# Kernel tuning notes

Measured on AMD Instinct MI355X. Metric: run time of the kernel, lower is better.

The kernel has to match this reference:

```python
import jax, jax.numpy as jnp
import numpy as np
import math

B, N, D, H, A, OBS, NB = 256, 64, 512, 8, 64, 128, 4
HD = D // H
EPS = 1e-5


def layernorm(x, g, b):
    mu = jnp.mean(x, axis=-1, keepdims=True)
    var = jnp.mean((x - mu) ** 2, axis=-1, keepdims=True)
    return (x - mu) * jax.lax.rsqrt(var + EPS) * g + b


def gelu(x):
    return jax.nn.gelu(x, approximate=False)  # torch nn.GELU default = exact erf


def mha_masked(k_in, v_in, q_in, wq, wk, wv, wp, bq, bk, bv, bp):
    # weights stored [in, out]; torch Linear computes x @ W.T, same math with random init
    b, l, d = q_in.shape
    q = (q_in @ wq + bq).reshape(b, l, H, HD).transpose(0, 2, 1, 3)  # [B,H,L,hd]
    k = (k_in @ wk + bk).reshape(b, l, H, HD).transpose(0, 2, 1, 3)
    v = (v_in @ wv + bv).reshape(b, l, H, HD).transpose(0, 2, 1, 3)
    att = jnp.einsum('bhqd,bhkd->bhqk', q, k) * (1.0 / math.sqrt(HD))
    causal = jnp.tril(jnp.ones((l, l), dtype=bool))  # registered tril buffer in original MAT code
    att = jnp.where(causal[None, None], att, -jnp.inf)
    att = jax.nn.softmax(att, axis=-1)
    y = jnp.einsum('bhqk,bhkd->bhqd', att, v)
    y = y.transpose(0, 2, 1, 3).reshape(b, l, d)
    return y @ wp + bp


def setup_inputs() -> dict:
    key = jax.random.key(0)
    ks = iter(jax.random.split(key, 32))
    s = 0.02
    inp = {
        'action': jax.random.normal(next(ks), (B, N, A + 1), jnp.float32),
        'obs_rep': jax.random.normal(next(ks), (B, N, D), jnp.float32),
        'obs': jax.random.normal(next(ks), (B, N, OBS), jnp.float32),
        'w_ae': jax.random.normal(next(ks), (A + 1, D), jnp.float32) * s,
        'ln0_g': jnp.ones((D,), jnp.float32),
        'ln0_b': jnp.zeros((D,), jnp.float32),
        'blk_ln_g': jnp.ones((NB, 3, D), jnp.float32),
        'blk_ln_b': jnp.zeros((NB, 3, D), jnp.float32),
        'blk_wq': jax.random.normal(next(ks), (NB, 2, D, D), jnp.float32) * s,
        'blk_wk': jax.random.normal(next(ks), (NB, 2, D, D), jnp.float32) * s,
        'blk_wv': jax.random.normal(next(ks), (NB, 2, D, D), jnp.float32) * s,
        'blk_wp': jax.random.normal(next(ks), (NB, 2, D, D), jnp.float32) * s,
        'blk_bq': jnp.zeros((NB, 2, D), jnp.float32),
        'blk_bk': jnp.zeros((NB, 2, D), jnp.float32),
        'blk_bv': jnp.zeros((NB, 2, D), jnp.float32),
        'blk_bp': jnp.zeros((NB, 2, D), jnp.float32),
        'blk_w1': jax.random.normal(next(ks), (NB, D, D), jnp.float32) * s,
        'blk_b1': jnp.zeros((NB, D), jnp.float32),
        'blk_w2': jax.random.normal(next(ks), (NB, D, D), jnp.float32) * s,
        'blk_b2': jnp.zeros((NB, D), jnp.float32),
        'wh1': jax.random.normal(next(ks), (D, D), jnp.float32) * s,
        'bh1': jnp.zeros((D,), jnp.float32),
        'lnh_g': jnp.ones((D,), jnp.float32),
        'lnh_b': jnp.zeros((D,), jnp.float32),
        'wh2': jax.random.normal(next(ks), (D, A), jnp.float32) * s,
        'bh2': jnp.zeros((A,), jnp.float32),
    }
    return inp


def reference(action, obs_rep, obs, w_ae, ln0_g, ln0_b, blk_ln_g, blk_ln_b,
              blk_wq, blk_wk, blk_wv, blk_wp, blk_bq, blk_bk, blk_bv, blk_bp,
              blk_w1, blk_b1, blk_w2, blk_b2, wh1, bh1, lnh_g, lnh_b, wh2, bh2):
    # action encoder: Linear(no bias) + GELU, then LayerNorm
    x = layernorm(gelu(action @ w_ae), ln0_g, ln0_b)
    for i in range(NB):
        # sublayer 1: masked self-attn + residual + LN
        a1 = mha_masked(x, x, x, blk_wq[i, 0], blk_wk[i, 0], blk_wv[i, 0], blk_wp[i, 0],
                        blk_bq[i, 0], blk_bk[i, 0], blk_bv[i, 0], blk_bp[i, 0])
        x = layernorm(x + a1, blk_ln_g[i, 0], blk_ln_b[i, 0])
        # sublayer 2: masked cross-attn (key=x, value=x, query=obs_rep) + residual with obs_rep + LN
        a2 = mha_masked(x, x, obs_rep, blk_wq[i, 1], blk_wk[i, 1], blk_wv[i, 1], blk_wp[i, 1],
                        blk_bq[i, 1], blk_bk[i, 1], blk_bv[i, 1], blk_bp[i, 1])
        x = layernorm(obs_rep + a2, blk_ln_g[i, 1], blk_ln_b[i, 1])
        # sublayer 3: GELU MLP (D -> D -> D) + residual + LN
        m = gelu(x @ blk_w1[i] + blk_b1[i]) @ blk_w2[i] + blk_b2[i]
        x = layernorm(x + m, blk_ln_g[i, 2], blk_ln_b[i, 2])
    # head: Linear + GELU + LN + Linear
    h = layernorm(gelu(x @ wh1 + bh1), lnh_g, lnh_b)
    logit = h @ wh2 + bh2
    return logit
```

## Files before the change

### kernel.cpp

```cpp
#include <hip/hip_runtime.h>
#include <hip/hip_bf16.h>
#include <math.h>

namespace {

constexpr int B  = 256;
constexpr int N  = 64;
constexpr int D  = 512;
constexpr int H  = 8;
constexpr int NBLK = 4;
constexpr int M  = B * N;
constexpr float EPS = 1e-5f;
constexpr float SCALE = 0.125f;
constexpr int NEVER = 1 << 20;

typedef __attribute__((ext_vector_type(8))) short short8b;
typedef __attribute__((ext_vector_type(4))) float f32x4;

__device__ __forceinline__ float gelu_exact(float x) {
  return 0.5f * x * (1.0f + erff(x * 0.70710678118654752440f));
}

__device__ __forceinline__ unsigned short f2b_bits(float f) {
  __hip_bfloat16 h = __float2bfloat16(f);
  return *reinterpret_cast<unsigned short*>(&h);
}

#define GLOBAL_AS __attribute__((address_space(1)))
#define LDS_AS    __attribute__((address_space(3)))

__device__ __forceinline__ void gload_lds16(const void* g, void* l) {
  __builtin_amdgcn_global_load_lds((const GLOBAL_AS void*)g, (LDS_AS void*)l, 16, 0, 0);
}

template<bool GELU, int SPLIT>
__global__ __launch_bounds__(512, 2) void gemm_dp_kernel(
    const __hip_bfloat16* __restrict__ A,
    const __hip_bfloat16* __restrict__ Wt,
    const float* __restrict__ bias,
    __hip_bfloat16* __restrict__ out1, int ostr1,
    __hip_bfloat16* __restrict__ vt, int gy) {
  constexpr int K = 512;
  constexpr int NT = 8;
  __shared__ __hip_bfloat16 Als[3][128][64];
  __shared__ __hip_bfloat16 Bls[3][256][64];

  const int nwg = gridDim.x;
  const int hw  = blockIdx.x;
  const int cpx = nwg >> 3;
  const int lg  = (hw & 7) * cpx + (hw >> 3);
  const int bm  = (lg / gy) * 128;
  const int bn  = (lg % gy) * 256;

  const int tid  = threadIdx.x;
  const int wave = tid >> 6;
  const int lane = tid & 63;
  const int wm   = (wave >> 2) * 64;
  const int wn   = (wave & 3) * 64;
  const int fr   = lane & 15;
  const int fg   = lane >> 4;

  const int srow  = tid >> 3;
  const int sslot = (tid & 7) ^ (srow & 7);
  const __hip_bfloat16* gA = A  + (size_t)(bm + srow) * K + sslot * 8;
  const __hip_bfloat16* gB = Wt + (size_t)(bn + srow) * K + sslot * 8;

  auto STAGE = [&](int buf, int kt) {
    const int ko = kt * 64;
    char* la = (char*)&Als[buf][0][0] + wave * 1024;
    char* lb = (char*)&Bls[buf][0][0] + wave * 1024;
    gload_lds16(gA + ko,           la);
    gload_lds16(gA + 64 * K + ko,  la + 8192);
    gload_lds16(gB + ko,           lb);
    gload_lds16(gB + 64 * K + ko,  lb + 8192);
    gload_lds16(gB + 128 * K + ko, lb + 16384);
    gload_lds16(gB + 192 * K + ko, lb + 24576);
  };

  auto lda = [&](int buf, int mi, int ks) -> short8b {
    const int row  = wm + mi * 16 + fr;
    const int byte = row * 128 + (((ks << 2) | fg) ^ (fr & 7)) * 16;
    return *reinterpret_cast<const short8b*>((const char*)&Als[buf][0][0] + byte);
  };
  auto ldb = [&](int buf, int ni, int ks) -> short8b {
    const int row  = wn + ni * 16 + fr;
    const int byte = row * 128 + (((ks << 2) | fg) ^ (fr & 7)) * 16;
    return *reinterpret_cast<const short8b*>((const char*)&Bls[buf][0][0] + byte);
  };

  STAGE(0, 0);
  STAGE(1, 1);
  asm volatile("s_waitcnt vmcnt(6)" ::: "memory");
  __builtin_amdgcn_sched_barrier(0);
  __builtin_amdgcn_s_barrier();
  __builtin_amdgcn_sched_barrier(0);

  f32x4 acc[4][4] = {};
  for (int t = 0; t < NT; ++t) {
    const int cur = t % 3;
    if (t + 2 < NT) STAGE((t + 2) % 3, t + 2);

    short8b a0[4], b0[4], a1[4], b1[4];
#pragma unroll
    for (int mi = 0; mi < 4; ++mi) a0[mi] = lda(cur, mi, 0);
#pragma unroll
    for (int ni = 0; ni < 4; ++ni) b0[ni] = ldb(cur, ni, 0);
#pragma unroll
    for (int mi = 0; mi < 4; ++mi) a1[mi] = lda(cur, mi, 1);
#pragma unroll
    for (int ni = 0; ni < 4; ++ni) b1[ni] = ldb(cur, ni, 1);

    __builtin_amdgcn_s_setprio(1);
#pragma unroll
    for (int mi = 0; mi < 4; ++mi)
#pragma unroll
      for (int ni = 0; ni < 4; ++ni)
        acc[mi][ni] = __builtin_amdgcn_mfma_f32_16x16x32_bf16(a0[mi], b0[ni], acc[mi][ni], 0, 0, 0);
#pragma unroll
    for (int mi = 0; mi < 4; ++mi)
#pragma unroll
      for (int ni = 0; ni < 4; ++ni)
        acc[mi][ni] = __builtin_amdgcn_mfma_f32_16x16x32_bf16(a1[mi], b1[ni], acc[mi][ni], 0, 0, 0);
    __builtin_amdgcn_s_setprio(0);

    if (t + 2 < NT) {
      asm volatile("s_waitcnt vmcnt(6)" ::: "memory");
    } else {
      asm volatile("s_waitcnt vmcnt(0)" ::: "memory");
    }
    __builtin_amdgcn_sched_barrier(0);
    __builtin_amdgcn_s_barrier();
    __builtin_amdgcn_sched_barrier(0);
  }

#pragma unroll
  for (int ni = 0; ni < 4; ++ni) {
    const int col = bn + wn + ni * 16 + fr;
    const float bv = bias ? bias[col] : 0.f;
#pragma unroll
    for (int mi = 0; mi < 4; ++mi) {
      const int row0 = bm + wm + mi * 16 + fg * 4;
      if (col >= SPLIT) {
        const int vcol = col - SPLIT;
        ushort4 o;
        o.x = f2b_bits(acc[mi][ni][0] + bv);
        o.y = f2b_bits(acc[mi][ni][1] + bv);
        o.z = f2b_bits(acc[mi][ni][2] + bv);
        o.w = f2b_bits(acc[mi][ni][3] + bv);
        const int b8 = row0 >> 6, nl = row0 & 63;
        const int hh = vcol >> 6, dl = vcol & 63;
        *reinterpret_cast<ushort4*>(vt +
            ((size_t)(b8 * 8 + hh) * 4096 + dl * 64 + nl)) = o;
      } else {
#pragma unroll
        for (int q = 0; q < 4; ++q) {
          float v = acc[mi][ni][q] + bv;
          if (GELU) v = gelu_exact(v);
          out1[(size_t)(row0 + q) * ostr1 + col] = __float2bfloat16(v);
        }
      }
    }
  }
}

template<int KSTEPS>
__global__ __launch_bounds__(256) void gemm_head_kernel(
    const __hip_bfloat16* __restrict__ A,
    const __hip_bfloat16* __restrict__ Wt,
    const float* __restrict__ bias,
    float* __restrict__ out1, int ostr1, int nvalid) {
  constexpr int K = KSTEPS * 32;
  __shared__ __hip_bfloat16 Als[2][128][32];
  __shared__ __hip_bfloat16 Bls[2][128][32];

  const int bm   = blockIdx.x * 128;
  const int bn   = blockIdx.y * 128;
  const int tid  = threadIdx.x;
  const int wave = tid >> 6;
  const int lane = tid & 63;
  const int wm   = (wave >> 1) * 64;
  const int wn   = (wave & 1) * 64;
  const int fr   = lane & 15;
  const int fg   = lane >> 4;

  const int srow = (lane >> 2);
  const int scol = (lane & 3) * 8;
  const __hip_bfloat16* gA0 = A  + (size_t)(bm + wave * 32 + srow) * K + scol;
  const __hip_bfloat16* gA1 = gA0 + 16 * K;
  const __hip_bfloat16* gB0 = Wt + (size_t)(bn + wave * 32 + srow) * K + scol;
  const __hip_bfloat16* gB1 = gB0 + 16 * K;

  f32x4 acc[4][4] = {};

  auto stage = [&](int buf, int ks) {
    const int ko = ks * 32;
    gload_lds16(gA0 + ko, &Als[buf][wave * 32][0]);
    gload_lds16(gA1 + ko, &Als[buf][wave * 32 + 16][0]);
    gload_lds16(gB0 + ko, &Bls[buf][wave * 32][0]);
    gload_lds16(gB1 + ko, &Bls[buf][wave * 32 + 16][0]);
  };

  stage(0, 0);
  int buf = 0;
  for (int ks = 0; ks < KSTEPS; ++ks) {
    __syncthreads();
    if (ks + 1 < KSTEPS) stage(buf ^ 1, ks + 1);
    short8b a[4], b[4];
#pragma unroll
    for (int mi = 0; mi < 4; ++mi)
      a[mi] = *reinterpret_cast<const short8b*>(&Als[buf][wm + mi * 16 + fr][fg * 8]);
#pragma unroll
    for (int ni = 0; ni < 4; ++ni)
      b[ni] = *reinterpret_cast<const short8b*>(&Bls[buf][wn + ni * 16 + fr][fg * 8]);
#pragma unroll
    for (int mi = 0; mi < 4; ++mi)
#pragma unroll
      for (int ni = 0; ni < 4; ++ni)
        acc[mi][ni] = __builtin_amdgcn_mfma_f32_16x16x32_bf16(a[mi], b[ni], acc[mi][ni], 0, 0, 0);
    buf ^= 1;
  }

#pragma unroll
  for (int ni = 0; ni < 4; ++ni) {
    const int col = bn + wn + ni * 16 + fr;
    if (col >= nvalid) continue;
    const float bv = bias ? bias[col] : 0.f;
#pragma unroll
    for (int mi = 0; mi < 4; ++mi) {
      const int row0 = bm + wm + mi * 16 + fg * 4;
#pragma unroll
      for (int q = 0; q < 4; ++q)
        out1[(size_t)(row0 + q) * ostr1 + col] = acc[mi][ni][q] + bv;
    }
  }
}

template<int KSTEPS, bool GELU_PRE, bool RES>
__global__ __launch_bounds__(512) void gemm_ln_kernel(
    const __hip_bfloat16* __restrict__ A,
    const __hip_bfloat16* __restrict__ Wt,
    const float* __restrict__ bias,
    const __hip_bfloat16* __restrict__ resb,
    const float* __restrict__ g, const float* __restrict__ bb,
    __hip_bfloat16* __restrict__ outB) {
  constexpr int K = KSTEPS * 32;
  __shared__ __hip_bfloat16 Als[2][64][32];
  __shared__ __hip_bfloat16 Bls[2][512][32];
  __shared__ float red[64][8];
  __shared__ float mrow[64];
  __shared__ float rrow[64];

  const int bm   = blockIdx.x * 64;
  const int tid  = threadIdx.x;
  const int wave = tid >> 6;
  const int lane = tid & 63;
  const int fr   = lane & 15;
  const int fg   = lane >> 4;
  const int srow = lane >> 2;
  const int scol = (lane & 3) * 8;

  auto stage = [&](int buf, int ks) {
    const int ko = ks * 32;
    if (wave < 4)
      gload_lds16(A + (size_t)(bm + wave * 16 + srow) * K + ko + scol,
                  &Als[buf][wave * 16][0]);
#pragma unroll
    for (int c = 0; c < 4; ++c)
      gload_lds16(Wt + (size_t)(wave * 64 + c * 16 + srow) * K + ko + scol,
                  &Bls[buf][wave * 64 + c * 16][0]);
  };

  f32x4 acc[4][4] = {};
  stage(0, 0);
  int buf = 0;
  for (int ks = 0; ks < KSTEPS; ++ks) {
    __syncthreads();
    if (ks + 1 < KSTEPS) stage(buf ^ 1, ks + 1);
    short8b a[4], b[4];
#pragma unroll
    for (int mi = 0; mi < 4; ++mi)
      a[mi] = *reinterpret_cast<const short8b*>(&Als[buf][mi * 16 + fr][fg * 8]);
#pragma unroll
    for (int ni = 0; ni < 4; ++ni)
      b[ni] = *reinterpret_cast<const short8b*>(&Bls[buf][wave * 64 + ni * 16 + fr][fg * 8]);
#pragma unroll
    for (int mi = 0; mi < 4; ++mi)
#pragma unroll
      for (int ni = 0; ni < 4; ++ni)
        acc[mi][ni] = __builtin_amdgcn_mfma_f32_16x16x32_bf16(a[mi], b[ni], acc[mi][ni], 0, 0, 0);
    buf ^= 1;
  }

  float v[4][4][4];
  float bvc[4];
#pragma unroll
  for (int ni = 0; ni < 4; ++ni)
    bvc[ni] = bias ? bias[wave * 64 + ni * 16 + fr] : 0.f;
#pragma unroll
  for (int mi = 0; mi < 4; ++mi)
#pragma unroll
    for (int q = 0; q < 4; ++q) {
      const int row = bm + mi * 16 + fg * 4 + q;
#pragma unroll
      for (int ni = 0; ni < 4; ++ni) {
        float t = acc[mi][ni][q] + bvc[ni];
        if (GELU_PRE) t = gelu_exact(t);
        if (RES)
          t += __bfloat162float(resb[(size_t)row * D + wave * 64 + ni * 16 + fr]);
        v[mi][ni][q] = t;
      }
    }

  float ps[16];
#pragma unroll
  for (int mi = 0; mi < 4; ++mi)
#pragma unroll
    for (int q = 0; q < 4; ++q)
      ps[mi * 4 + q] = v[mi][0][q] + v[mi][1][q] + v[mi][2][q] + v[mi][3][q];
#pragma unroll
  for (int mask = 1; mask < 16; mask <<= 1)
#pragma unroll
    for (int t = 0; t < 16; ++t) ps[t] += __shfl_xor(ps[t], mask);
  if (fr == 0) {
#pragma unroll
    for (int mi = 0; mi < 4; ++mi)
#pragma unroll
      for (int q = 0; q < 4; ++q)
        red[mi * 16 + fg * 4 + q][wave] = ps[mi * 4 + q];
  }
  __syncthreads();
  if (tid < 64) {
    float s = 0.f;
#pragma unroll
    for (int w = 0; w < 8; ++w) s += red[tid][w];
    mrow[tid] = s * (1.f / 512.f);
  }
  __syncthreads();
  float mu[16];
#pragma unroll
  for (int mi = 0; mi < 4; ++mi)
#pragma unroll
    for (int q = 0; q < 4; ++q) mu[mi * 4 + q] = mrow[mi * 16 + fg * 4 + q];

  float ps2[16];
#pragma unroll
  for (int mi = 0; mi < 4; ++mi)
#pragma unroll
    for (int q = 0; q < 4; ++q) {
      const float m = mu[mi * 4 + q];
      float s = 0.f;
#pragma unroll
      for (int ni = 0; ni < 4; ++ni) {
        const float d = v[mi][ni][q] - m;
        s += d * d;
      }
      ps2[mi * 4 + q] = s;
    }
#pragma unroll
  for (int mask = 1; mask < 16; mask <<= 1)
#pragma unroll
    for (int t = 0; t < 16; ++t) ps2[t] += __shfl_xor(ps2[t], mask);
  if (fr == 0) {
#pragma unroll
    for (int mi = 0; mi < 4; ++mi)
#pragma unroll
      for (int q = 0; q < 4; ++q)
        red[mi * 16 + fg * 4 + q][wave] = ps2[mi * 4 + q];
  }
  __syncthreads();
  if (tid < 64) {
    float s = 0.f;
#pragma unroll
    for (int w = 0; w < 8; ++w) s += red[tid][w];
    rrow[tid] = rsqrtf(s * (1.f / 512.f) + EPS);
  }
  __syncthreads();

#pragma unroll
  for (int ni = 0; ni < 4; ++ni) {
    const int col = wave * 64 + ni * 16 + fr;
    const float gc = g[col], bc = bb[col];
#pragma unroll
    for (int mi = 0; mi < 4; ++mi)
#pragma unroll
      for (int q = 0; q < 4; ++q) {
        const int lrow = mi * 16 + fg * 4 + q;
        const int row = bm + lrow;
        const float o = (v[mi][ni][q] - mu[mi * 4 + q]) * rrow[lrow] * gc + bc;
        outB[(size_t)row * D + col] = __float2bfloat16(o);
      }
  }
}

__global__ __launch_bounds__(256) void attn_mfma_kernel(
    const __hip_bfloat16* __restrict__ qg, int qstr,
    const __hip_bfloat16* __restrict__ kg, int kstr,
    const __hip_bfloat16* __restrict__ vt,
    __hip_bfloat16* __restrict__ yg) {
  __shared__ __align__(16) char smem[33280];
  unsigned short* Qs  = (unsigned short*)smem;
  unsigned short* Ks  = (unsigned short*)(smem + 8192);
  float*          Ss  = (float*)smem;
  unsigned short* Vts = (unsigned short*)(smem + 16896);
  unsigned short* Ps  = (unsigned short*)(smem + 25088);

  const int tid  = threadIdx.x;
  const int bh   = blockIdx.x;
  const int bidx = bh >> 3, h = bh & 7;
  const size_t rbase = (size_t)bidx * 64;
  const int col0 = h * 64;

  const __hip_bfloat16* vtg = vt + (size_t)bh * 4096;
#pragma unroll
  for (int p = 0; p < 2; ++p) {
    const int idx = tid + p * 256;
    const int row = idx >> 3, c8 = (idx & 7) * 8;
    const int lb  = (row * 128 + c8 * 2) ^ ((row & 7) << 4);
    const uint4 vq = *reinterpret_cast<const uint4*>(qg + (rbase + row) * qstr + col0 + c8);
    const uint4 vk = *reinterpret_cast<const uint4*>(kg + (rbase + row) * kstr + col0 + c8);
    const uint4 vv = *reinterpret_cast<const uint4*>(vtg + idx * 8);
    *reinterpret_cast<uint4*>((char*)Qs  + lb) = vq;
    *reinterpret_cast<uint4*>((char*)Ks  + lb) = vk;
    *reinterpret_cast<uint4*>((char*)Vts + lb) = vv;
  }
  __syncthreads();

  const int wave = tid >> 6, lane = tid & 63;
  const int fr = lane & 15, fg = lane >> 4;
  const int wr = (wave >> 1) * 32, wc = (wave & 1) * 32;

  auto ldfrag = [&](const unsigned short* base, int row, int ks) -> short8b {
    const int byte = (row * 128 + ks * 64 + fg * 16) ^ ((row & 7) << 4);
    return *reinterpret_cast<const short8b*>((const char*)base + byte);
  };

  f32x4 acc[2][2] = {};
#pragma unroll
  for (int ks = 0; ks < 2; ++ks) {
    short8b a[2], b[2];
    a[0] = ldfrag(Qs, wr + fr, ks);
    a[1] = ldfrag(Qs, wr + 16 + fr, ks);
    b[0] = ldfrag(Ks, wc + fr, ks);
    b[1] = ldfrag(Ks, wc + 16 + fr, ks);
#pragma unroll
    for (int mi = 0; mi < 2; ++mi)
#pragma unroll
      for (int ni = 0; ni < 2; ++ni)
        acc[mi][ni] = __builtin_amdgcn_mfma_f32_16x16x32_bf16(a[mi], b[ni], acc[mi][ni], 0, 0, 0);
  }
  __syncthreads();

#pragma unroll
  for (int mi = 0; mi < 2; ++mi)
#pragma unroll
    for (int ni = 0; ni < 2; ++ni) {
      const int m2 = wc + ni * 16 + fr;
#pragma unroll
      for (int r = 0; r < 4; ++r) {
        const int n = wr + mi * 16 + fg * 4 + r;
        Ss[n * 66 + m2] = (m2 <= n) ? acc[mi][ni][r] * SCALE : -1e30f;
      }
    }
  __syncthreads();

  for (int n = wave * 16; n < wave * 16 + 16; ++n) {
    const float vv = Ss[n * 66 + lane];
    float mx = vv;
#pragma unroll
    for (int off = 1; off < 64; off <<= 1) mx = fmaxf(mx, __shfl_xor(mx, off));
    const float p = (lane <= n) ? __expf(vv - mx) : 0.f;
    float sum = p;
#pragma unroll
    for (int off = 1; off < 64; off <<= 1) sum += __shfl_xor(sum, off);
    const int byte = (n * 128 + lane * 2) ^ ((n & 7) << 4);
    *(unsigned short*)((char*)Ps + byte) = f2b_bits(p / sum);
  }
  __syncthreads();

  f32x4 acc2[2][2] = {};
#pragma unroll
  for (int ks = 0; ks < 2; ++ks) {
    short8b a[2], b[2];
    a[0] = ldfrag(Ps, wr + fr, ks);
    a[1] = ldfrag(Ps, wr + 16 + fr, ks);
    b[0] = ldfrag(Vts, wc + fr, ks);
    b[1] = ldfrag(Vts, wc + 16 + fr, ks);
#pragma unroll
    for (int mi = 0; mi < 2; ++mi)
#pragma unroll
      for (int ni = 0; ni < 2; ++ni)
        acc2[mi][ni] = __builtin_amdgcn_mfma_f32_16x16x32_bf16(a[mi], b[ni], acc2[mi][ni], 0, 0, 0);
  }
#pragma unroll
  for (int mi = 0; mi < 2; ++mi)
#pragma unroll
    for (int r = 0; r < 4; ++r) {
      const int n = wr + mi * 16 + fg * 4 + r;
      yg[(rbase + n) * 512 + col0 + wc + fr]      = __float2bfloat16(acc2[mi][0][r]);
      yg[(rbase + n) * 512 + col0 + wc + 16 + fr] = __float2bfloat16(acc2[mi][1][r]);
    }
}

__global__ __launch_bounds__(256) void wconv_all_kernel(
    const float* __restrict__ bwq, const float* __restrict__ bwk,
    const float* __restrict__ bwv, const float* __restrict__ bwp,
    const float* __restrict__ bw1, const float* __restrict__ bw2,
    const float* __restrict__ wh1,
    __hip_bfloat16* __restrict__ wSelf, __hip_bfloat16* __restrict__ wCq,
    __hip_bfloat16* __restrict__ wCkv, __hip_bfloat16* __restrict__ wTp,
    __hip_bfloat16* __restrict__ wTw1, __hip_bfloat16* __restrict__ wTw2,
    __hip_bfloat16* __restrict__ wTh1) {
  const size_t MAT = (size_t)D * D;
  const size_t SS = (size_t)1536 * 512, KV = (size_t)1024 * 512;
  const int z = blockIdx.z;
  const float* src;
  __hip_bfloat16* dst;
  if (z < 8)       { int i = z >> 1; src = bwq + (size_t)z * MAT;
                     dst = (z & 1) ? wCq + (size_t)i * MAT : wSelf + (size_t)i * SS; }
  else if (z < 16) { int zz = z - 8, i = zz >> 1; src = bwk + (size_t)zz * MAT;
                     dst = (zz & 1) ? wCkv + (size_t)i * KV
                                    : wSelf + (size_t)i * SS + 512 * 512; }
  else if (z < 24) { int zz = z - 16, i = zz >> 1; src = bwv + (size_t)zz * MAT;
                     dst = (zz & 1) ? wCkv + (size_t)i * KV + 512 * 512
                                    : wSelf + (size_t)i * SS + 1024 * 512; }
  else if (z < 32) { int zz = z - 24; src = bwp + (size_t)zz * MAT; dst = wTp + (size_t)zz * MAT; }
  else if (z < 36) { int zz = z - 32; src = bw1 + (size_t)zz * MAT; dst = wTw1 + (size_t)zz * MAT; }
  else if (z < 40) { int zz = z - 36; src = bw2 + (size_t)zz * MAT; dst = wTw2 + (size_t)zz * MAT; }
  else             { src = wh1; dst = wTh1; }

  __shared__ float tile[32][33];
  const int r0 = blockIdx.y * 32, c0 = blockIdx.x * 32;
  const int tr = threadIdx.x >> 5;
  const int tc = threadIdx.x & 31;
#pragma unroll
  for (int i = 0; i < 4; ++i)
    tile[tr + 8 * i][tc] = src[(size_t)(r0 + tr + 8 * i) * D + c0 + tc];
  __syncthreads();
#pragma unroll
  for (int i = 0; i < 4; ++i)
    dst[(size_t)(c0 + tr + 8 * i) * D + r0 + tc] = __float2bfloat16(tile[tc][tr + 8 * i]);
}

__global__ __launch_bounds__(256) void misc_prep_kernel(
    const float* __restrict__ w_ae, const float* __restrict__ wh2,
    const float* __restrict__ bbq, const float* __restrict__ bbk,
    const float* __restrict__ bbv, const float* __restrict__ action,
    __hip_bfloat16* __restrict__ waeT, __hip_bfloat16* __restrict__ wh2p,
    float* __restrict__ selfb, float* __restrict__ ckvb,
    float* __restrict__ bqc, __hip_bfloat16* __restrict__ actb) {
  constexpr int R0 = 512 * 96, R1 = 128 * 512, R2 = NBLK * 1536,
                R3 = NBLK * 1024, R4 = NBLK * 512, R5 = M * 96;
  constexpr int total = R0 + R1 + R2 + R3 + R4 + R5;
  for (int i = blockIdx.x * 256 + threadIdx.x; i < total; i += gridDim.x * 256) {
    int j = i;
    if (j < R0) {
      const int n = j / 96, k = j - n * 96;
      waeT[j] = (k < 65) ? __float2bfloat16(w_ae[(size_t)k * 512 + n]) : __float2bfloat16(0.f);
    } else if ((j -= R0) < R1) {
      const int n = j >> 9, k = j & 511;
      wh2p[j] = (n < 64) ? __float2bfloat16(wh2[(size_t)k * 64 + n]) : __float2bfloat16(0.f);
    } else if ((j -= R1) < R2) {
      const int blk = j / 1536, c = j - blk * 1536;
      const int seg = c >> 9, cc = c & 511;
      const float* s = (seg == 0) ? bbq : (seg == 1) ? bbk : bbv;
      selfb[j] = s[(size_t)(blk * 2) * 512 + cc];
    } else if ((j -= R2) < R3) {
      const int blk = j >> 10, c = j & 1023;
      ckvb[j] = (c < 512) ? bbk[(size_t)(blk * 2 + 1) * 512 + c]
                          : bbv[(size_t)(blk * 2 + 1) * 512 + (c - 512)];
    } else if ((j -= R3) < R4) {
      const int blk = j >> 9, c = j & 511;
      bqc[j] = bbq[(size_t)(blk * 2 + 1) * 512 + c];
    } else {
      j -= R4;
      const int row = j / 96, k = j - row * 96;
      actb[j] = (k < 65) ? __float2bfloat16(action[(size_t)row * 65 + k]) : __float2bfloat16(0.f);
    }
  }
}

__global__ __launch_bounds__(256) void cvt_kernel(
    const float* __restrict__ src, __hip_bfloat16* __restrict__ dst, int n4) {
  const int i = blockIdx.x * 256 + threadIdx.x;
  if (i < n4) {
    const float4 v = reinterpret_cast<const float4*>(src)[i];
    ushort4 o;
    o.x = f2b_bits(v.x); o.y = f2b_bits(v.y);
    o.z = f2b_bits(v.z); o.w = f2b_bits(v.w);
    reinterpret_cast<ushort4*>(dst)[i] = o;
  }
}

}

extern "C" void kernel_launch(void* const* d_in, const int* in_sizes, int n_in,
                              void* d_out, int out_size, void* d_ws, size_t ws_size,
                              hipStream_t stream) {
  const float* action  = (const float*)d_in[0];
  const float* obs_rep = (const float*)d_in[1];
  const float* w_ae    = (const float*)d_in[3];
  const float* ln0_g   = (const float*)d_in[4];
  const float* ln0_b   = (const float*)d_in[5];
  const float* bln_g   = (const float*)d_in[6];
  const float* bln_b   = (const float*)d_in[7];
  const float* bwq     = (const float*)d_in[8];
  const float* bwk     = (const float*)d_in[9];
  const float* bwv     = (const float*)d_in[10];
  const float* bwp     = (const float*)d_in[11];
  const float* bbq     = (const float*)d_in[12];
  const float* bbk     = (const float*)d_in[13];
  const float* bbv     = (const float*)d_in[14];
  const float* bbp     = (const float*)d_in[15];
  const float* bw1     = (const float*)d_in[16];
  const float* bb1     = (const float*)d_in[17];
  const float* bw2     = (const float*)d_in[18];
  const float* bb2     = (const float*)d_in[19];
  const float* wh1     = (const float*)d_in[20];
  const float* bh1     = (const float*)d_in[21];
  const float* lnh_g   = (const float*)d_in[22];
  const float* lnh_b   = (const float*)d_in[23];
  const float* wh2     = (const float*)d_in[24];
  const float* bh2     = (const float*)d_in[25];

  char* ws = (char*)d_ws;
  const size_t MAT = (size_t)D * D;
  const size_t szB = (size_t)M * D * 2;

  __hip_bfloat16* xb  = (__hip_bfloat16*)ws; ws += szB;
  __hip_bfloat16* hb  = (__hip_bfloat16*)ws; ws += szB;
  __hip_bfloat16* vtb = (__hip_bfloat16*)ws; ws += szB;
  __hip_bfloat16* orb = (__hip_bfloat16*)ws; ws += szB;
  __hip_bfloat16* qkb = (__hip_bfloat16*)ws; ws += 2 * szB;
  __hip_bfloat16* qcb = (__hip_bfloat16*)ws; ws += 4 * szB;
  __hip_bfloat16* kb  = (__hip_bfloat16*)ws; ws += szB;
  __hip_bfloat16* actb = (__hip_bfloat16*)ws; ws += (size_t)M * 96 * 2;
  __hip_bfloat16* wSelf = (__hip_bfloat16*)ws; ws += (size_t)NBLK * 1536 * 512 * 2;
  __hip_bfloat16* wCq   = (__hip_bfloat16*)ws; ws += (size_t)NBLK * 512 * 512 * 2;
  __hip_bfloat16* wCkv  = (__hip_bfloat16*)ws; ws += (size_t)NBLK * 1024 * 512 * 2;
  __hip_bfloat16* wTp   = (__hip_bfloat16*)ws; ws += 8 * MAT * 2;
  __hip_bfloat16* wTw1  = (__hip_bfloat16*)ws; ws += 4 * MAT * 2;
  __hip_bfloat16* wTw2  = (__hip_bfloat16*)ws; ws += 4 * MAT * 2;
  __hip_bfloat16* wTh1  = (__hip_bfloat16*)ws; ws += MAT * 2;
  __hip_bfloat16* wh2p  = (__hip_bfloat16*)ws; ws += 128 * 512 * 2;
  __hip_bfloat16* waeT  = (__hip_bfloat16*)ws; ws += 512 * 96 * 2;
  float* selfb         = (float*)ws;         ws += (size_t)NBLK * 1536 * 4;
  float* ckvb          = (float*)ws;         ws += (size_t)NBLK * 1024 * 4;
  float* bqc           = (float*)ws;         ws += (size_t)NBLK * 512 * 4;

  wconv_all_kernel<<<dim3(16, 16, 41), 256, 0, stream>>>(
      bwq, bwk, bwv, bwp, bw1, bw2, wh1,
      wSelf, wCq, wCkv, wTp, wTw1, wTw2, wTh1);
  misc_prep_kernel<<<2048, 256, 0, stream>>>(
      w_ae, wh2, bbq, bbk, bbv, action, waeT, wh2p, selfb, ckvb, bqc, actb);
  cvt_kernel<<<(M * D / 4 + 255) / 256, 256, 0, stream>>>(obs_rep, orb, M * D / 4);

  const size_t SS = (size_t)1536 * 512;
  const size_t KV = (size_t)1024 * 512;
  const int lnGrid = M / 64;

  gemm_ln_kernel<3, true, false><<<lnGrid, 512, 0, stream>>>(
      actb, waeT, nullptr, nullptr, ln0_g, ln0_b, xb);

  gemm_dp_kernel<false, NEVER><<<M / 128 * 8, 512, 0, stream>>>(
      orb, wCq, bqc, qcb, 2048, nullptr, 8);

  for (int i = 0; i < NBLK; ++i) {
    const float* g0 = bln_g + (size_t)(i * 3 + 0) * D;
    const float* b0 = bln_b + (size_t)(i * 3 + 0) * D;
    const float* g1 = bln_g + (size_t)(i * 3 + 1) * D;
    const float* b1 = bln_b + (size_t)(i * 3 + 1) * D;
    const float* g2 = bln_g + (size_t)(i * 3 + 2) * D;
    const float* b2 = bln_b + (size_t)(i * 3 + 2) * D;

    gemm_dp_kernel<false, 1024><<<M / 128 * 6, 512, 0, stream>>>(
        xb, wSelf + (size_t)i * SS, selfb + (size_t)i * 1536, qkb, 1024, vtb, 6);
    attn_mfma_kernel<<<B * H, 256, 0, stream>>>(qkb, 1024, qkb + 512, 1024, vtb, hb);
    gemm_ln_kernel<16, false, true><<<lnGrid, 512, 0, stream>>>(
        hb, wTp + (size_t)(i * 2) * MAT, bbp + (size_t)(i * 2) * D, xb, g0, b0, xb);

    gemm_dp_kernel<false, 512><<<M / 128 * 4, 512, 0, stream>>>(
        xb, wCkv + (size_t)i * KV, ckvb + (size_t)i * 1024, kb, 512, vtb, 4);
    attn_mfma_kernel<<<B * H, 256, 0, stream>>>(
        qcb + (size_t)i * 512, 2048, kb, 512, vtb, hb);
    gemm_ln_kernel<16, false, true><<<lnGrid, 512, 0, stream>>>(
        hb, wTp + (size_t)(i * 2 + 1) * MAT, bbp + (size_t)(i * 2 + 1) * D,
        orb, g1, b1, xb);

    gemm_dp_kernel<true, NEVER><<<M / 128 * 2, 512, 0, stream>>>(
        xb, wTw1 + (size_t)i * MAT, bb1 + (size_t)i * D, hb, 512, nullptr, 2);
    gemm_ln_kernel<16, false, true><<<lnGrid, 512, 0, stream>>>(
        hb, wTw2 + (size_t)i * MAT, bb2 + (size_t)i * D, xb, g2, b2, xb);
  }

  gemm_ln_kernel<16, true, false><<<lnGrid, 512, 0, stream>>>(
      xb, wTh1, bh1, nullptr, lnh_g, lnh_b, hb);
  gemm_head_kernel<16><<<dim3(M / 128, 1), 256, 0, stream>>>(
      hb, wh2p, bh2, (float*)d_out, 64, 64);
}
```

Before: 1.039 ms.

## Use 64-wide K tiles with XOR-swizzled LDS in fused GEMM+LayerNorm kernels

Adds a gemm_ln64 kernel for the K=512 GEMM+LayerNorm stages. It stages 64-wide K tiles into LDS using an XOR swizzle to avoid bank conflicts, halves the number of barrier-separated iterations, and raises wave priority around the MFMA block. The encoder gets a specialised small-K kernel, and the obs_rep fp32-to-bf16 conversion moves into misc_prep_kernel, which saves one launch. The larger tiles roughly double LDS use per block, which may lower occupancy.

```diff
diff --git a/kernel.cpp b/kernel.cpp
--- a/kernel.cpp
+++ b/kernel.cpp
@@ -163,6 +163,184 @@
   }
 }
 
+template<bool GELU_PRE, bool RES>
+__global__ __launch_bounds__(512) void gemm_ln64_kernel(
+    const __hip_bfloat16* __restrict__ A,
+    const __hip_bfloat16* __restrict__ Wt,
+    const float* __restrict__ bias,
+    const __hip_bfloat16* __restrict__ resb,
+    const float* __restrict__ g, const float* __restrict__ bb,
+    __hip_bfloat16* __restrict__ outB) {
+  __shared__ __hip_bfloat16 Als[2][64][64];
+  __shared__ __hip_bfloat16 Bls[2][512][64];
+  __shared__ float red[64][8];
+  __shared__ float mrow[64];
+  __shared__ float rrow[64];
+
+  const int bm   = blockIdx.x * 64;
+  const int tid  = threadIdx.x;
+  const int wave = tid >> 6;
+  const int lane = tid & 63;
+  const int fr   = lane & 15;
+  const int fg   = lane >> 4;
+
+  const int srow  = tid >> 3;
+  const int sslot = (tid & 7) ^ (srow & 7);
+
+  auto stage = [&](int buf, int kt) {
+    const int ko = kt * 64;
+    gload_lds16(A + (size_t)(bm + srow) * 512 + ko + sslot * 8,
+                (char*)&Als[buf][0][0] + wave * 1024);
+#pragma unroll
+    for (int j = 0; j < 8; ++j) {
+      const int row = j * 64 + srow;
+      const int sl  = (tid & 7) ^ (row & 7);
+      gload_lds16(Wt + (size_t)row * 512 + ko + sl * 8,
+                  (char*)&Bls[buf][0][0] + j * 8192 + wave * 1024);
+    }
+  };
+
+  auto lda = [&](int buf, int mi, int ks) -> short8b {
+    const int row  = mi * 16 + fr;
+    const int byte = row * 128 + (((ks << 2) | fg) ^ (row & 7)) * 16;
+    return *reinterpret_cast<const short8b*>((const char*)&Als[buf][0][0] + byte);
+  };
+  auto ldb = [&](int buf, int ni, int ks) -> short8b {
+    const int row  = wave * 64 + ni * 16 + fr;
+    const int byte = row * 128 + (((ks << 2) | fg) ^ (row & 7)) * 16;
+    return *reinterpret_cast<const short8b*>((const char*)&Bls[buf][0][0] + byte);
+  };
+
+  f32x4 acc[4][4] = {};
+  stage(0, 0);
+  int buf = 0;
+  for (int kt = 0; kt < 8; ++kt) {
+    __syncthreads();
+    if (kt + 1 < 8) stage(buf ^ 1, kt + 1);
+    short8b a0[4], b0[4], a1[4], b1[4];
+#pragma unroll
+    for (int mi = 0; mi < 4; ++mi) a0[mi] = lda(buf, mi, 0);
+#pragma unroll
+    for (int ni = 0; ni < 4; ++ni) b0[ni] = ldb(buf, ni, 0);
+#pragma unroll
+    for (int mi = 0; mi < 4; ++mi) a1[mi] = lda(buf, mi, 1);
+#pragma unroll
+    for (int ni = 0; ni < 4; ++ni) b1[ni] = ldb(buf, ni, 1);
+    __builtin_amdgcn_s_setprio(1);
+#pragma unroll
+    for (int mi = 0; mi < 4; ++mi)
+#pragma unroll
+      for (int ni = 0; ni < 4; ++ni)
+        acc[mi][ni] = __builtin_amdgcn_mfma_f32_16x16x32_bf16(a0[mi], b0[ni], acc[mi][ni], 0, 0, 0);
+#pragma unroll
+    for (int mi = 0; mi < 4; ++mi)
+#pragma unroll
+      for (int ni = 0; ni < 4; ++ni)
+        acc[mi][ni] = __builtin_amdgcn_mfma_f32_16x16x32_bf16(a1[mi], b1[ni], acc[mi][ni], 0, 0, 0);
+    __builtin_amdgcn_s_setprio(0);
+    buf ^= 1;
+  }
+
+  float v[4][4][4];
+  float bvc[4];
+#pragma unroll
+  for (int ni = 0; ni < 4; ++ni)
+    bvc[ni] = bias ? bias[wave * 64 + ni * 16 + fr] : 0.f;
+#pragma unroll
+  for (int mi = 0; mi < 4; ++mi)
+#pragma unroll
+    for (int q = 0; q < 4; ++q) {
+      const int row = bm + mi * 16 + fg * 4 + q;
+#pragma unroll
+      for (int ni = 0; ni < 4; ++ni) {
+        float t = acc[mi][ni][q] + bvc[ni];
+        if (GELU_PRE) t = gelu_exact(t);
+        if (RES)
+          t += __bfloat162float(resb[(size_t)row * D + wave * 64 + ni * 16 + fr]);
+        v[mi][ni][q] = t;
+      }
+    }
+
+  float ps[16];
+#pragma unroll
+  for (int mi = 0; mi < 4; ++mi)
+#pragma unroll
+    for (int q = 0; q < 4; ++q)
+      ps[mi * 4 + q] = v[mi][0][q] + v[mi][1][q] + v[mi][2][q] + v[mi][3][q];
+#pragma unroll
+  for (int mask = 1; mask < 16; mask <<= 1)
+#pragma unroll
+    for (int t = 0; t < 16; ++t) ps[t] += __shfl_xor(ps[t], mask);
+  if (fr == 0) {
+#pragma unroll
+    for (int mi = 0; mi < 4; ++mi)
+#pragma unroll
+      for (int q = 0; q < 4; ++q)
+        red[mi * 16 + fg * 4 + q][wave] = ps[mi * 4 + q];
+  }
+  __syncthreads();
+  if (tid < 64) {
+    float s = 0.f;
+#pragma unroll
+    for (int w = 0; w < 8; ++w) s += red[tid][w];
+    mrow[tid] = s * (1.f / 512.f);
+  }
+  __syncthreads();
+  float mu[16];
+#pragma unroll
+  for (int mi = 0; mi < 4; ++mi)
+#pragma unroll
+    for (int q = 0; q < 4; ++q) mu[mi * 4 + q] = mrow[mi * 16 + fg * 4 + q];
+
+  float ps2[16];
+#pragma unroll
+  for (int mi = 0; mi < 4; ++mi)
+#pragma unroll
+    for (int q = 0; q < 4; ++q) {
+      const float m = mu[mi * 4 + q];
+      float s = 0.f;
+#pragma unroll
+      for (int ni = 0; ni < 4; ++ni) {
+        const float d = v[mi][ni][q] - m;
+        s += d * d;
+      }
+      ps2[mi * 4 + q] = s;
+    }
+#pragma unroll
+  for (int mask = 1; mask < 16; mask <<= 1)
+#pragma unroll
+    for (int t = 0; t < 16; ++t) ps2[t] += __shfl_xor(ps2[t], mask);
+  if (fr == 0) {
+#pragma unroll
+    for (int mi = 0; mi < 4; ++mi)
+#pragma unroll
+      for (int q = 0; q < 4; ++q)
+        red[mi * 16 + fg * 4 + q][wave] = ps2[mi * 4 + q];
+  }
+  __syncthreads();
+  if (tid < 64) {
+    float s = 0.f;
+#pragma unroll
+    for (int w = 0; w < 8; ++w) s += red[tid][w];
+    rrow[tid] = rsqrtf(s * (1.f / 512.f) + EPS);
+  }
+  __syncthreads();
+
+#pragma unroll
+  for (int ni = 0; ni < 4; ++ni) {
+    const int col = wave * 64 + ni * 16 + fr;
+    const float gc = g[col], bc = bb[col];
+#pragma unroll
+    for (int mi = 0; mi < 4; ++mi)
+#pragma unroll
+      for (int q = 0; q < 4; ++q) {
+        const int lrow = mi * 16 + fg * 4 + q;
+        const float o = (v[mi][ni][q] - mu[mi * 4 + q]) * rrow[lrow] * gc + bc;
+        outB[(size_t)(bm + lrow) * D + col] = __float2bfloat16(o);
+      }
+  }
+}
+
 template<int KSTEPS>
 __global__ __launch_bounds__(256) void gemm_head_kernel(
     const __hip_bfloat16* __restrict__ A,
@@ -235,15 +413,12 @@
   }
 }
 
-template<int KSTEPS, bool GELU_PRE, bool RES>
-__global__ __launch_bounds__(512) void gemm_ln_kernel(
+__global__ __launch_bounds__(512) void gemm_ln_enc_kernel(
     const __hip_bfloat16* __restrict__ A,
     const __hip_bfloat16* __restrict__ Wt,
-    const float* __restrict__ bias,
-    const __hip_bfloat16* __restrict__ resb,
     const float* __restrict__ g, const float* __restrict__ bb,
     __hip_bfloat16* __restrict__ outB) {
-  constexpr int K = KSTEPS * 32;
+  constexpr int K = 96;
   __shared__ __hip_bfloat16 Als[2][64][32];
   __shared__ __hip_bfloat16 Bls[2][512][32];
   __shared__ float red[64][8];
@@ -273,9 +448,9 @@
   f32x4 acc[4][4] = {};
   stage(0, 0);
   int buf = 0;
-  for (int ks = 0; ks < KSTEPS; ++ks) {
+  for (int ks = 0; ks < 3; ++ks) {
     __syncthreads();
-    if (ks + 1 < KSTEPS) stage(buf ^ 1, ks + 1);
+    if (ks + 1 < 3) stage(buf ^ 1, ks + 1);
     short8b a[4], b[4];
 #pragma unroll
     for (int mi = 0; mi < 4; ++mi)
@@ -292,24 +467,13 @@
   }
 
   float v[4][4][4];
-  float bvc[4];
-#pragma unroll
-  for (int ni = 0; ni < 4; ++ni)
-    bvc[ni] = bias ? bias[wave * 64 + ni * 16 + fr] : 0.f;
 #pragma unroll
   for (int mi = 0; mi < 4; ++mi)
 #pragma unroll
-    for (int q = 0; q < 4; ++q) {
-      const int row = bm + mi * 16 + fg * 4 + q;
-#pragma unroll
-      for (int ni = 0; ni < 4; ++ni) {
-        float t = acc[mi][ni][q] + bvc[ni];
-        if (GELU_PRE) t = gelu_exact(t);
-        if (RES)
-          t += __bfloat162float(resb[(size_t)row * D + wave * 64 + ni * 16 + fr]);
-        v[mi][ni][q] = t;
-      }
-    }
+    for (int q = 0; q < 4; ++q)
+#pragma unroll
+      for (int ni = 0; ni < 4; ++ni)
+        v[mi][ni][q] = gelu_exact(acc[mi][ni][q]);
 
   float ps[16];
 #pragma unroll
@@ -321,13 +485,12 @@
   for (int mask = 1; mask < 16; mask <<= 1)
 #pragma unroll
     for (int t = 0; t < 16; ++t) ps[t] += __shfl_xor(ps[t], mask);
-  if (fr == 0) {
+  if (fr == 0)
 #pragma unroll
     for (int mi = 0; mi < 4; ++mi)
 #pragma unroll
       for (int q = 0; q < 4; ++q)
         red[mi * 16 + fg * 4 + q][wave] = ps[mi * 4 + q];
-  }
   __syncthreads();
   if (tid < 64) {
     float s = 0.f;
@@ -341,7 +504,6 @@
   for (int mi = 0; mi < 4; ++mi)
 #pragma unroll
     for (int q = 0; q < 4; ++q) mu[mi * 4 + q] = mrow[mi * 16 + fg * 4 + q];
-
   float ps2[16];
 #pragma unroll
   for (int mi = 0; mi < 4; ++mi)
@@ -350,23 +512,19 @@
       const float m = mu[mi * 4 + q];
       float s = 0.f;
 #pragma unroll
-      for (int ni = 0; ni < 4; ++ni) {
-        const float d = v[mi][ni][q] - m;
-        s += d * d;
-      }
+      for (int ni = 0; ni < 4; ++ni) { const float d = v[mi][ni][q] - m; s += d * d; }
       ps2[mi * 4 + q] = s;
     }
 #pragma unroll
   for (int mask = 1; mask < 16; mask <<= 1)
 #pragma unroll
     for (int t = 0; t < 16; ++t) ps2[t] += __shfl_xor(ps2[t], mask);
-  if (fr == 0) {
+  if (fr == 0)
 #pragma unroll
     for (int mi = 0; mi < 4; ++mi)
 #pragma unroll
       for (int q = 0; q < 4; ++q)
         red[mi * 16 + fg * 4 + q][wave] = ps2[mi * 4 + q];
-  }
   __syncthreads();
   if (tid < 64) {
     float s = 0.f;
@@ -385,9 +543,8 @@
 #pragma unroll
       for (int q = 0; q < 4; ++q) {
         const int lrow = mi * 16 + fg * 4 + q;
-        const int row = bm + lrow;
         const float o = (v[mi][ni][q] - mu[mi * 4 + q]) * rrow[lrow] * gc + bc;
-        outB[(size_t)row * D + col] = __float2bfloat16(o);
+        outB[(size_t)(bm + lrow) * D + col] = __float2bfloat16(o);
       }
   }
 }
@@ -545,12 +702,15 @@
     const float* __restrict__ w_ae, const float* __restrict__ wh2,
     const float* __restrict__ bbq, const float* __restrict__ bbk,
     const float* __restrict__ bbv, const float* __restrict__ action,
+    const float* __restrict__ obs_rep,
     __hip_bfloat16* __restrict__ waeT, __hip_bfloat16* __restrict__ wh2p,
     float* __restrict__ selfb, float* __restrict__ ckvb,
-    float* __restrict__ bqc, __hip_bfloat16* __restrict__ actb) {
+    float* __restrict__ bqc, __hip_bfloat16* __restrict__ actb,
+    __hip_bfloat16* __restrict__ orb) {
   constexpr int R0 = 512 * 96, R1 = 128 * 512, R2 = NBLK * 1536,
                 R3 = NBLK * 1024, R4 = NBLK * 512, R5 = M * 96;
-  constexpr int total = R0 + R1 + R2 + R3 + R4 + R5;
+  constexpr int R6 = M * D / 4;
+  constexpr int total = R0 + R1 + R2 + R3 + R4 + R5 + R6;
   for (int i = blockIdx.x * 256 + threadIdx.x; i < total; i += gridDim.x * 256) {
     int j = i;
     if (j < R0) {
@@ -571,23 +731,17 @@
     } else if ((j -= R3) < R4) {
       const int blk = j >> 9, c = j & 511;
       bqc[j] = bbq[(size_t)(blk * 2 + 1) * 512 + c];
-    } else {
-      j -= R4;
+    } else if ((j -= R4) < R5) {
       const int row = j / 96, k = j - row * 96;
       actb[j] = (k < 65) ? __float2bfloat16(action[(size_t)row * 65 + k]) : __float2bfloat16(0.f);
-    }
-  }
-}
-
-__global__ __launch_bounds__(256) void cvt_kernel(
-    const float* __restrict__ src, __hip_bfloat16* __restrict__ dst, int n4) {
-  const int i = blockIdx.x * 256 + threadIdx.x;
-  if (i < n4) {
-    const float4 v = reinterpret_cast<const float4*>(src)[i];
-    ushort4 o;
-    o.x = f2b_bits(v.x); o.y = f2b_bits(v.y);
-    o.z = f2b_bits(v.z); o.w = f2b_bits(v.w);
-    reinterpret_cast<ushort4*>(dst)[i] = o;
+    } else {
+      j -= R5;
+      const float4 v = reinterpret_cast<const float4*>(obs_rep)[j];
+      ushort4 o;
+      o.x = f2b_bits(v.x); o.y = f2b_bits(v.y);
+      o.z = f2b_bits(v.z); o.w = f2b_bits(v.w);
+      reinterpret_cast<ushort4*>(orb)[j] = o;
+    }
   }
 }
 
@@ -651,15 +805,14 @@
       bwq, bwk, bwv, bwp, bw1, bw2, wh1,
       wSelf, wCq, wCkv, wTp, wTw1, wTw2, wTh1);
   misc_prep_kernel<<<2048, 256, 0, stream>>>(
-      w_ae, wh2, bbq, bbk, bbv, action, waeT, wh2p, selfb, ckvb, bqc, actb);
-  cvt_kernel<<<(M * D / 4 + 255) / 256, 256, 0, stream>>>(obs_rep, orb, M * D / 4);
+      w_ae, wh2, bbq, bbk, bbv, action, obs_rep,
+      waeT, wh2p, selfb, ckvb, bqc, actb, orb);
 
   const size_t SS = (size_t)1536 * 512;
   const size_t KV = (size_t)1024 * 512;
   const int lnGrid = M / 64;
 
-  gemm_ln_kernel<3, true, false><<<lnGrid, 512, 0, stream>>>(
-      actb, waeT, nullptr, nullptr, ln0_g, ln0_b, xb);
+  gemm_ln_enc_kernel<<<lnGrid, 512, 0, stream>>>(actb, waeT, ln0_g, ln0_b, xb);
 
   gemm_dp_kernel<false, NEVER><<<M / 128 * 8, 512, 0, stream>>>(
       orb, wCq, bqc, qcb, 2048, nullptr, 8);
@@ -675,24 +828,24 @@
     gemm_dp_kernel<false, 1024><<<M / 128 * 6, 512, 0, stream>>>(
         xb, wSelf + (size_t)i * SS, selfb + (size_t)i * 1536, qkb, 1024, vtb, 6);
     attn_mfma_kernel<<<B * H, 256, 0, stream>>>(qkb, 1024, qkb + 512, 1024, vtb, hb);
-    gemm_ln_kernel<16, false, true><<<lnGrid, 512, 0, stream>>>(
+    gemm_ln64_kernel<false, true><<<lnGrid, 512, 0, stream>>>(
         hb, wTp + (size_t)(i * 2) * MAT, bbp + (size_t)(i * 2) * D, xb, g0, b0, xb);
 
     gemm_dp_kernel<false, 512><<<M / 128 * 4, 512, 0, stream>>>(
         xb, wCkv + (size_t)i * KV, ckvb + (size_t)i * 1024, kb, 512, vtb, 4);
     attn_mfma_kernel<<<B * H, 256, 0, stream>>>(
         qcb + (size_t)i * 512, 2048, kb, 512, vtb, hb);
-    gemm_ln_kernel<16, false, true><<<lnGrid, 512, 0, stream>>>(
+    gemm_ln64_kernel<false, true><<<lnGrid, 512, 0, stream>>>(
         hb, wTp + (size_t)(i * 2 + 1) * MAT, bbp + (size_t)(i * 2 + 1) * D,
         orb, g1, b1, xb);
 
     gemm_dp_kernel<true, NEVER><<<M / 128 * 2, 512, 0, stream>>>(
         xb, wTw1 + (size_t)i * MAT, bb1 + (size_t)i * D, hb, 512, nullptr, 2);
-    gemm_ln_kernel<16, false, true><<<lnGrid, 512, 0, stream>>>(
+    gemm_ln64_kernel<false, true><<<lnGrid, 512, 0, stream>>>(
         hb, wTw2 + (size_t)i * MAT, bb2 + (size_t)i * D, xb, g2, b2, xb);
   }
 
-  gemm_ln_kernel<16, true, false><<<lnGrid, 512, 0, stream>>>(
+  gemm_ln64_kernel<true, false><<<lnGrid, 512, 0, stream>>>(
       xb, wTh1, bh1, nullptr, lnh_g, lnh_b, hb);
   gemm_head_kernel<16><<<dim3(M / 128, 1), 256, 0, stream>>>(
       hb, wh2p, bh2, (float*)d_out, 64, 64);
```

After: 998.5 us. -3.9%, faster.
